# Performance work log

Hardware: AMD Instinct MI355X
Metric: run time of the kernel (lower is better)

Reference implementation:

```python
import jax, jax.numpy as jnp
import numpy as np

N_ITER = 10
TOL = 1e-05
EPS_R = 1e-10
REG = 1e-06
F32_EPS = float(np.finfo(np.float32).eps)


def setup_inputs() -> dict:
    key = jax.random.key(0)
    K, T, F, _ = 6, 2048, 513, 2
    X = jax.random.normal(key, (K, T, F, 2), dtype=jnp.float32)
    return {"X": X}


def _aux_iva_iss(X):
    # X: (K, T, F, 2) real/imag -> complex (F, K, T)
    Xc = (X[..., 0] + 1j * X[..., 1]).astype(jnp.complex64)
    Xc = jnp.transpose(Xc, (2, 0, 1))  # (F, K, T)
    F, K, T = Xc.shape
    eyeK = jnp.eye(K, dtype=jnp.complex64)
    W = jnp.broadcast_to(eyeK, (F, K, K)).astype(jnp.complex64)  # (F, K, K)
    Xh = jnp.conj(Xc)
    done = jnp.array(False)

    for _ in range(N_ITER):
        W_old = W
        # demix: Y[f] = W[f] @ X[f]
        Y = jnp.einsum('fkm,fmt->fkt', W, Xc)
        # per-(source, frame) norms across frequency
        r = jnp.sqrt(jnp.clip(jnp.sum(jnp.abs(Y) ** 2, axis=0), EPS_R))  # (K, T)
        wt = 1.0 / jnp.clip(r, EPS_R)  # laplace contrast g'(r)/r
        # weighted covariances V[f,k] = (X_f * wt[k]) X_f^H / T + reg*I  -> (F, K, K, K)
        V = jnp.einsum('fat,kt,fbt->fkab', Xc, wt.astype(jnp.complex64), Xh) / T
        V = V + REG * eyeK
        # sequential ISS updates over target row k (vectorized over f, m)
        for k in range(K):
            wk = W[:, k, :]  # (F, K)
            wk_c = jnp.conj(wk)
            quad = jnp.einsum('fa,fmab,fb->fm', wk, V, wk_c)  # w_k V_m w_k^H
            denom = jnp.clip(quad.real, EPS_R)  # (F, K)
            num = jnp.einsum('fma,fmab,fb->fm', W, V, wk_c)  # w_m V_m w_k^H
            vk = num / denom  # (F, K)
            vk = vk.at[:, k].set((1.0 - 1.0 / jnp.sqrt(denom[:, k])).astype(jnp.complex64))
            W = W - vk[:, :, None] * wk[:, None, :]
        # emulate early-break on relative change (freeze W once converged)
        W = jnp.where(done, W_old, W)
        diff = jnp.linalg.norm((W - W_old).reshape(-1))
        rel = diff / jnp.clip(jnp.linalg.norm(W_old.reshape(-1)), F32_EPS)
        done = jnp.logical_or(done, rel < TOL)

    Y = jnp.einsum('fkm,fmt->fkt', W, Xc)  # (F, K, T)
    # ref_mic == 0 -> no projection-back rescaling
    Y_out = jnp.transpose(Y, (1, 2, 0))  # (K, T, F)
    return jnp.stack([Y_out.real, Y_out.imag], axis=-1)  # (K, T, F, 2)


def reference(X):
    return _aux_iva_iss(X)
```

## Files before the change

kernel.cpp:

```cpp
#include <hip/hip_runtime.h>
#include <hip/hip_bf16.h>
#include <math.h>

#define T_DIM 2048
#define F_DIM 513
#define N_ITER 10

#define OFF_W0   0
#define OFF_W1   36936
#define OFF_P0   73872
#define OFF_P1   74898
#define OFF_RA0  75924
#define OFF_RA1  88212
#define OFF_VP   100500

typedef __attribute__((ext_vector_type(8))) short bf16x8;
typedef __attribute__((ext_vector_type(4))) float f32x4;

static __device__ inline unsigned pack2bf(float a, float b) {
    union { __hip_bfloat16 h; unsigned short u; } ca, cb;
    ca.h = __float2bfloat16(a);
    cb.h = __float2bfloat16(b);
    return (unsigned)ca.u | ((unsigned)cb.u << 16);
}

static __device__ inline void scatterV(float* V6, int e, float sum) {
    if (e < 6) {
        V6[(e * 6 + e) * 2]     = sum + 1e-6f;
        V6[(e * 6 + e) * 2 + 1] = 0.f;
    } else if (e < 21) {
        int p = e - 6;
        int a = (p < 1) ? 1 : (p < 3) ? 2 : (p < 6) ? 3 : (p < 10) ? 4 : 5;
        int b = p - a * (a - 1) / 2;
        V6[(a * 6 + b) * 2] = sum;
        V6[(b * 6 + a) * 2] = sum;
    } else {
        int p = e - 21;
        int a = (p < 1) ? 1 : (p < 3) ? 2 : (p < 6) ? 3 : (p < 10) ? 4 : 5;
        int b = p - a * (a - 1) / 2;
        V6[(a * 6 + b) * 2 + 1] =  sum;
        V6[(b * 6 + a) * 2 + 1] = -sum;
    }
}

__global__ __launch_bounds__(256) void transp(const float2* __restrict__ X,
                                              float2* __restrict__ Xt,
                                              float* __restrict__ ws) {
    const int fb  = blockIdx.x + 64 * (blockIdx.y + 17 * blockIdx.z);
    const int tid = threadIdx.x;
    if (fb < 73) {
        int idx = fb * 256 + tid;
        if (idx < F_DIM * 36) {
            int e = idx % 36;
            ws[OFF_W0 + 2 * idx]     = ((e / 6) == (e % 6)) ? 1.0f : 0.0f;
            ws[OFF_W0 + 2 * idx + 1] = 0.0f;
        }
    } else if (fb < 78) {
        int idx = (fb - 73) * 256 + tid;
        if (idx < 2 * F_DIM) { ws[OFF_P0 + idx] = 1.0f; ws[OFF_P1 + idx] = 1.0f; }
    } else if (fb < 126) {
        int idx = (fb - 78) * 256 + tid;
        if (idx < 12288) ws[OFF_RA0 + idx] = 0.0f;
    }

    __shared__ float2 tile[32][33];
    const int k  = blockIdx.z;
    const int t0 = blockIdx.x * 32;
    const int f0 = blockIdx.y * 32;
    const int tx = tid & 31, ty = tid >> 5;
#pragma unroll
    for (int j = 0; j < 4; ++j) {
        int t = t0 + ty + j * 8;
        int f = f0 + tx;
        if (f < F_DIM) tile[ty + j * 8][tx] = X[((size_t)k * T_DIM + t) * F_DIM + f];
    }
    __syncthreads();
#pragma unroll
    for (int j = 0; j < 4; ++j) {
        int f = f0 + ty + j * 8;
        int t = t0 + tx;
        if (f < F_DIM) Xt[((size_t)f * 6 + k) * T_DIM + t] = tile[tx][ty + j * 8];
    }
}

__global__ __launch_bounds__(256) void passA1C(const float2* __restrict__ Xt,
                                               float* __restrict__ ws,
                                               const float* __restrict__ pin,
                                               float* __restrict__ pout,
                                               const float* __restrict__ wOld,
                                               float* __restrict__ wNew,
                                               float* __restrict__ r2acc,
                                               int do_iss) {
    __shared__ float Wl[16][72];
    __shared__ float VL[16][432];
    __shared__ float sc[8];
    const int tid = threadIdx.x, wv = tid >> 6, lane = tid & 63;
    const int tc = blockIdx.x, fc = blockIdx.y;

    bool frozen;
    {
        float d2 = 0.f, o2 = 0.f;
        for (int i = tid; i < F_DIM; i += 256) { d2 += pin[2 * i]; o2 += pin[2 * i + 1]; }
#pragma unroll
        for (int d = 1; d < 64; d <<= 1) { d2 += __shfl_xor(d2, d); o2 += __shfl_xor(o2, d); }
        if (lane == 0) { sc[wv * 2] = d2; sc[wv * 2 + 1] = o2; }
        __syncthreads();
        d2 = sc[0] + sc[2] + sc[4] + sc[6];
        o2 = sc[1] + sc[3] + sc[5] + sc[7];
        float rel = sqrtf(d2) / fmaxf(sqrtf(o2), 1.1920929e-07f);
        frozen = (rel < 1e-5f);
        __syncthreads();
    }

    const int fl = wv * 4 + (lane >> 4);
    const int f  = fc * 16 + fl;
    const int m  = lane & 15;
    const bool act = (f < F_DIM) && (m < 6);

    if (do_iss == 0) {
        if (act) {
            const float* Wp = wOld + ((size_t)f * 36 + m * 6) * 2;
#pragma unroll
            for (int a = 0; a < 6; ++a) {
                Wl[fl][(m * 6 + a) * 2]     = Wp[2 * a];
                Wl[fl][(m * 6 + a) * 2 + 1] = Wp[2 * a + 1];
            }
        }
    } else if (frozen) {
        if (act) {
            const float* Wp = wOld + ((size_t)f * 36 + m * 6) * 2;
            float* Wq = wNew + ((size_t)f * 36 + m * 6) * 2;
#pragma unroll
            for (int a = 0; a < 6; ++a) {
                float v0 = Wp[2 * a], v1 = Wp[2 * a + 1];
                Wq[2 * a] = v0; Wq[2 * a + 1] = v1;
                Wl[fl][(m * 6 + a) * 2] = v0; Wl[fl][(m * 6 + a) * 2 + 1] = v1;
            }
        }
        if (tc == 0 && m == 0 && f < F_DIM) { pout[2 * f] = 0.f; pout[2 * f + 1] = 1.f; }
    } else {
        if (f < F_DIM) {
            const float* vp = ws + OFF_VP + (size_t)f * 4 * 216;
            for (int v = m; v < 216; v += 16) {
                float sum = (vp[v] + vp[216 + v] + vp[432 + v] + vp[648 + v]) * (1.0f / (float)T_DIM);
                scatterV(&VL[fl][(v / 36) * 72], v % 36, sum);
            }
        }
        __syncthreads();
        float w6[6][2], wo6[6][2];
#pragma unroll
        for (int a = 0; a < 6; ++a) { w6[a][0] = 0.f; w6[a][1] = 0.f; wo6[a][0] = 0.f; wo6[a][1] = 0.f; }
        if (act) {
            const float* Wp = wOld + ((size_t)f * 36 + m * 6) * 2;
#pragma unroll
            for (int a = 0; a < 6; ++a) {
                w6[a][0] = Wp[2 * a]; w6[a][1] = Wp[2 * a + 1];
                wo6[a][0] = w6[a][0]; wo6[a][1] = w6[a][1];
            }
        }
        const float2* Vm = (const float2*)&VL[fl][0];
        for (int kk = 0; kk < 6; ++kk) {
            float wk[6][2];
#pragma unroll
            for (int a = 0; a < 6; ++a) {
                wk[a][0] = __shfl(w6[a][0], kk, 16);
                wk[a][1] = __shfl(w6[a][1], kk, 16);
            }
            if (act) {
                float t6[6][2];
#pragma unroll
                for (int a = 0; a < 6; ++a) {
                    float tr = 0.f, ti = 0.f;
#pragma unroll
                    for (int b = 0; b < 6; ++b) {
                        float2 vv = Vm[m * 36 + a * 6 + b];
                        tr += vv.x * wk[b][0] + vv.y * wk[b][1];
                        ti += vv.y * wk[b][0] - vv.x * wk[b][1];
                    }
                    t6[a][0] = tr; t6[a][1] = ti;
                }
                float quad = 0.f, nr = 0.f, ni = 0.f;
#pragma unroll
                for (int a = 0; a < 6; ++a) {
                    quad += wk[a][0] * t6[a][0] - wk[a][1] * t6[a][1];
                    nr   += w6[a][0] * t6[a][0] - w6[a][1] * t6[a][1];
                    ni   += w6[a][0] * t6[a][1] + w6[a][1] * t6[a][0];
                }
                float denom = fmaxf(quad, 1e-10f);
                float vkr, vki;
                if (m == kk) { vkr = 1.0f - 1.0f / sqrtf(denom); vki = 0.0f; }
                else { float inv = 1.0f / denom; vkr = nr * inv; vki = ni * inv; }
#pragma unroll
                for (int a = 0; a < 6; ++a) {
                    w6[a][0] -= vkr * wk[a][0] - vki * wk[a][1];
                    w6[a][1] -= vkr * wk[a][1] + vki * wk[a][0];
                }
            }
        }
        float d2 = 0.f, o2 = 0.f;
        if (act) {
            float* Wq = wNew + ((size_t)f * 36 + m * 6) * 2;
#pragma unroll
            for (int a = 0; a < 6; ++a) {
                Wq[2 * a] = w6[a][0]; Wq[2 * a + 1] = w6[a][1];
                Wl[fl][(m * 6 + a) * 2] = w6[a][0]; Wl[fl][(m * 6 + a) * 2 + 1] = w6[a][1];
                float dr = w6[a][0] - wo6[a][0], di = w6[a][1] - wo6[a][1];
                d2 += dr * dr + di * di;
                o2 += wo6[a][0] * wo6[a][0] + wo6[a][1] * wo6[a][1];
            }
        }
#pragma unroll
        for (int d = 1; d < 8; d <<= 1) {
            d2 += __shfl_xor(d2, d);
            o2 += __shfl_xor(o2, d);
        }
        if (tc == 0 && m == 0 && f < F_DIM) { pout[2 * f] = d2; pout[2 * f + 1] = o2; }
    }
    __syncthreads();
    if (do_iss && frozen) return;

    float* r2s = &VL[0][0];
    const int t2 = tc * 128 + lane * 2;
    float acc[6][2];
#pragma unroll
    for (int k = 0; k < 6; ++k) { acc[k][0] = 0.f; acc[k][1] = 0.f; }
#pragma unroll
    for (int i = 0; i < 4; ++i) {
        const int ff = fc * 16 + wv * 4 + i;
        if (ff < F_DIM) {
            const float2* xf = Xt + (size_t)ff * 6 * T_DIM;
            float4 x4[6];
#pragma unroll
            for (int mm = 0; mm < 6; ++mm)
                x4[mm] = *(const float4*)(xf + (size_t)mm * T_DIM + t2);
            const float* wrow = Wl[wv * 4 + i];
#pragma unroll
            for (int k = 0; k < 6; ++k) {
                float y0r = 0.f, y0i = 0.f, y1r = 0.f, y1i = 0.f;
#pragma unroll
                for (int mm = 0; mm < 6; ++mm) {
                    float wr = wrow[(k * 6 + mm) * 2], wi = wrow[(k * 6 + mm) * 2 + 1];
                    y0r += wr * x4[mm].x - wi * x4[mm].y;
                    y0i += wr * x4[mm].y + wi * x4[mm].x;
                    y1r += wr * x4[mm].z - wi * x4[mm].w;
                    y1i += wr * x4[mm].w + wi * x4[mm].z;
                }
                acc[k][0] += y0r * y0r + y0i * y0i;
                acc[k][1] += y1r * y1r + y1i * y1i;
            }
        }
    }
    __syncthreads();
#pragma unroll
    for (int k = 0; k < 6; ++k) {
        r2s[(wv * 6 + k) * 128 + lane * 2]     = acc[k][0];
        r2s[(wv * 6 + k) * 128 + lane * 2 + 1] = acc[k][1];
    }
    __syncthreads();
    for (int v = tid; v < 768; v += 256) {
        int k = v >> 7, l = v & 127;
        float s = r2s[(0 * 6 + k) * 128 + l] + r2s[(1 * 6 + k) * 128 + l]
                + r2s[(2 * 6 + k) * 128 + l] + r2s[(3 * 6 + k) * 128 + l];
        atomicAdd(&r2acc[k * T_DIM + tc * 128 + l], s);
    }
}

__global__ __launch_bounds__(384) void passB(const float2* __restrict__ Xt,
                                             float* __restrict__ ws,
                                             const float* __restrict__ pin,
                                             const float* __restrict__ r2in,
                                             float* __restrict__ r2zero) {
    __shared__ __align__(16) char plane[16 * 528];
    __shared__ __align__(16) float gbuf[6][256];
    __shared__ float sc[12];
    const int tid = threadIdx.x, wv = tid >> 6, lane = tid & 63;
    const int f = blockIdx.x, tq = blockIdx.y;

    {
        float d2 = 0.f, o2 = 0.f;
        for (int i = tid; i < F_DIM; i += 384) { d2 += pin[2 * i]; o2 += pin[2 * i + 1]; }
#pragma unroll
        for (int d = 1; d < 64; d <<= 1) { d2 += __shfl_xor(d2, d); o2 += __shfl_xor(o2, d); }
        if (lane == 0) { sc[wv * 2] = d2; sc[wv * 2 + 1] = o2; }
        __syncthreads();
        d2 = 0.f; o2 = 0.f;
#pragma unroll
        for (int w = 0; w < 6; ++w) { d2 += sc[w * 2]; o2 += sc[w * 2 + 1]; }
        float rel = sqrtf(d2) / fmaxf(sqrtf(o2), 1.1920929e-07f);
        __syncthreads();
        if (rel < 1e-5f) return;
    }

    {
        int bb = (f * 4 + tq) * 6;
#pragma unroll
        for (int i = 0; i < 6; ++i) {
            int idx = bb + i;
            if (idx < 12288) r2zero[idx] = 0.f;
        }
    }

    const float2* xb = Xt + (size_t)f * 6 * T_DIM;

    for (int i = tid; i < 528; i += 384) ((unsigned*)(plane + 12 * 528))[i] = 0;

    f32x4 acc0 = {0.f, 0.f, 0.f, 0.f};
    f32x4 acc1 = {0.f, 0.f, 0.f, 0.f};
    const int rc = lane & 15;
    const int G  = lane >> 4;
    const char* pu = plane + rc * 528 + G * 16;
    const float* gk = &gbuf[wv][0] + G * 8;

    for (int c = 0; c < 2; ++c) {
        const int t0 = tq * 512 + c * 256;
        __syncthreads();
        for (int i = tid; i < 1536; i += 384) {
            int kk = i >> 8, toff = i & 255;
            float s = r2in[kk * T_DIM + t0 + toff];
            float r = sqrtf(fmaxf(s, 1e-10f));
            gbuf[kk][toff] = 1.0f / fmaxf(r, 1e-10f);
        }
        for (int it = tid; it < 768; it += 384) {
            int mm = it >> 7, q = it & 127;
            float4 xv = *(const float4*)(xb + (size_t)mm * T_DIM + t0 + 2 * q);
            *(unsigned*)(plane + mm * 528 + 4 * q)       = pack2bf(xv.x, xv.z);
            *(unsigned*)(plane + (6 + mm) * 528 + 4 * q) = pack2bf(xv.y, xv.w);
        }
        __syncthreads();
#pragma unroll
        for (int s = 0; s < 8; ++s) {
            bf16x8 b = *(const bf16x8*)(pu + s * 64);
            f32x4 gA = *(const f32x4*)(gk + s * 32);
            f32x4 gB = *(const f32x4*)(gk + s * 32 + 4);
            const unsigned* bu = (const unsigned*)&b;
            bf16x8 a;
            unsigned* au = (unsigned*)&a;
            au[0] = pack2bf(__uint_as_float(bu[0] << 16) * gA[0],
                            __uint_as_float(bu[0] & 0xffff0000u) * gA[1]);
            au[1] = pack2bf(__uint_as_float(bu[1] << 16) * gA[2],
                            __uint_as_float(bu[1] & 0xffff0000u) * gA[3]);
            au[2] = pack2bf(__uint_as_float(bu[2] << 16) * gB[0],
                            __uint_as_float(bu[2] & 0xffff0000u) * gB[1]);
            au[3] = pack2bf(__uint_as_float(bu[3] << 16) * gB[2],
                            __uint_as_float(bu[3] & 0xffff0000u) * gB[3]);
            if (s & 1) acc1 = __builtin_amdgcn_mfma_f32_16x16x32_bf16(a, b, acc1, 0, 0, 0);
            else       acc0 = __builtin_amdgcn_mfma_f32_16x16x32_bf16(a, b, acc0, 0, 0, 0);
        }
    }
    __syncthreads();

    float* S = (float*)plane;
    {
        float* Sk = S + wv * 256;
#pragma unroll
        for (int r = 0; r < 4; ++r)
            Sk[(4 * G + r) * 16 + rc] = acc0[r] + acc1[r];
    }
    __syncthreads();

    if (tid < 216) {
        const int kk = tid / 36, e = tid % 36;
        const float* Sk = S + kk * 256;
        float val;
        if (e < 6) {
            val = Sk[e * 16 + e] + Sk[(6 + e) * 16 + (6 + e)];
        } else if (e < 21) {
            int p = e - 6;
            int a = (p < 1) ? 1 : (p < 3) ? 2 : (p < 6) ? 3 : (p < 10) ? 4 : 5;
            int b = p - a * (a - 1) / 2;
            val = Sk[a * 16 + b] + Sk[(6 + a) * 16 + (6 + b)];
        } else {
            int p = e - 21;
            int a = (p < 1) ? 1 : (p < 3) ? 2 : (p < 6) ? 3 : (p < 10) ? 4 : 5;
            int b = p - a * (a - 1) / 2;
            val = Sk[(6 + a) * 16 + b] - Sk[a * 16 + (6 + b)];
        }
        ws[OFF_VP + ((size_t)f * 4 + tq) * 216 + tid] = val;
    }
}

__global__ __launch_bounds__(64) void passC(float* __restrict__ ws,
                                            const float* __restrict__ pin,
                                            float* __restrict__ pout,
                                            const float* __restrict__ wOld,
                                            float* __restrict__ wNew) {
    __shared__ float VL[432];
    const int f = blockIdx.x;
    const int lane = threadIdx.x;
    {
        float d2 = 0.f, o2 = 0.f;
        for (int i = lane; i < F_DIM; i += 64) { d2 += pin[2 * i]; o2 += pin[2 * i + 1]; }
#pragma unroll
        for (int d = 1; d < 64; d <<= 1) { d2 += __shfl_xor(d2, d); o2 += __shfl_xor(o2, d); }
        float rel = sqrtf(d2) / fmaxf(sqrtf(o2), 1.1920929e-07f);
        if (rel < 1e-5f) {
            for (int v = lane; v < 72; v += 64)
                wNew[(size_t)f * 72 + v] = wOld[(size_t)f * 72 + v];
            if (lane == 0) { pout[2 * f] = 0.0f; pout[2 * f + 1] = 1.0f; }
            return;
        }
    }
    {
        const float* vp = ws + OFF_VP + (size_t)f * 4 * 216;
        for (int v = lane; v < 216; v += 64) {
            float sum = (vp[v] + vp[216 + v] + vp[432 + v] + vp[648 + v]) * (1.0f / (float)T_DIM);
            scatterV(&VL[(v / 36) * 72], v % 36, sum);
        }
    }
    __syncthreads();

    const int m = lane;
    const bool act = (m < 6);
    float w6[6][2], wo6[6][2];
#pragma unroll
    for (int a = 0; a < 6; ++a) { w6[a][0] = 0.f; w6[a][1] = 0.f; wo6[a][0] = 0.f; wo6[a][1] = 0.f; }
    if (act) {
        const float* Wp = wOld + ((size_t)f * 36 + m * 6) * 2;
#pragma unroll
        for (int a = 0; a < 6; ++a) {
            w6[a][0] = Wp[2 * a]; w6[a][1] = Wp[2 * a + 1];
            wo6[a][0] = w6[a][0]; wo6[a][1] = w6[a][1];
        }
    }
    const float2* Vm = (const float2*)VL;
    for (int kk = 0; kk < 6; ++kk) {
        float wk[6][2];
#pragma unroll
        for (int a = 0; a < 6; ++a) {
            wk[a][0] = __shfl(w6[a][0], kk);
            wk[a][1] = __shfl(w6[a][1], kk);
        }
        if (act) {
            float t6[6][2];
#pragma unroll
            for (int a = 0; a < 6; ++a) {
                float tr = 0.f, ti = 0.f;
#pragma unroll
                for (int b = 0; b < 6; ++b) {
                    float2 vv = Vm[m * 36 + a * 6 + b];
                    tr += vv.x * wk[b][0] + vv.y * wk[b][1];
                    ti += vv.y * wk[b][0] - vv.x * wk[b][1];
                }
                t6[a][0] = tr; t6[a][1] = ti;
            }
            float quad = 0.f, nr = 0.f, ni = 0.f;
#pragma unroll
            for (int a = 0; a < 6; ++a) {
                quad += wk[a][0] * t6[a][0] - wk[a][1] * t6[a][1];
                nr   += w6[a][0] * t6[a][0] - w6[a][1] * t6[a][1];
                ni   += w6[a][0] * t6[a][1] + w6[a][1] * t6[a][0];
            }
            float denom = fmaxf(quad, 1e-10f);
            float vkr, vki;
            if (m == kk) { vkr = 1.0f - 1.0f / sqrtf(denom); vki = 0.0f; }
            else { float inv = 1.0f / denom; vkr = nr * inv; vki = ni * inv; }
#pragma unroll
            for (int a = 0; a < 6; ++a) {
                w6[a][0] -= vkr * wk[a][0] - vki * wk[a][1];
                w6[a][1] -= vkr * wk[a][1] + vki * wk[a][0];
            }
        }
    }
    float d2 = 0.f, o2 = 0.f;
    if (act) {
        float* Wq = wNew + ((size_t)f * 36 + m * 6) * 2;
#pragma unroll
        for (int a = 0; a < 6; ++a) {
            Wq[2 * a] = w6[a][0]; Wq[2 * a + 1] = w6[a][1];
            float dr = w6[a][0] - wo6[a][0], di = w6[a][1] - wo6[a][1];
            d2 += dr * dr + di * di;
            o2 += wo6[a][0] * wo6[a][0] + wo6[a][1] * wo6[a][1];
        }
    }
#pragma unroll
    for (int d = 1; d < 8; d <<= 1) {
        d2 += __shfl_xor(d2, d);
        o2 += __shfl_xor(o2, d);
    }
    if (lane == 0) {
        pout[2 * f]     = d2;
        pout[2 * f + 1] = o2;
    }
}

__global__ __launch_bounds__(256) void finalY(const float2* __restrict__ X,
                                              const float* __restrict__ ws,
                                              float2* __restrict__ out) {
    const int f  = blockIdx.y * 256 + threadIdx.x;
    const int t0 = blockIdx.x * 4;
    if (f >= F_DIM) return;
    const float2* Wf = (const float2*)(ws + OFF_W0) + (size_t)f * 36;
    float2 w[36];
#pragma unroll
    for (int i = 0; i < 36; ++i) w[i] = Wf[i];
#pragma unroll
    for (int tl = 0; tl < 4; ++tl) {
        int t = t0 + tl;
        float2 x[6];
#pragma unroll
        for (int m = 0; m < 6; ++m) x[m] = X[((size_t)m * T_DIM + t) * F_DIM + f];
#pragma unroll
        for (int k = 0; k < 6; ++k) {
            float yr = 0.f, yi = 0.f;
#pragma unroll
            for (int m = 0; m < 6; ++m) {
                float2 wk = w[k * 6 + m];
                yr += wk.x * x[m].x - wk.y * x[m].y;
                yi += wk.x * x[m].y + wk.y * x[m].x;
            }
            out[((size_t)k * T_DIM + t) * F_DIM + f] = make_float2(yr, yi);
        }
    }
}

extern "C" void kernel_launch(void* const* d_in, const int* in_sizes, int n_in,
                              void* d_out, int out_size, void* d_ws, size_t ws_size,
                              hipStream_t stream) {
    (void)in_sizes; (void)n_in; (void)out_size; (void)ws_size;
    const float2* X = (const float2*)d_in[0];
    float* ws = (float*)d_ws;
    float2* out = (float2*)d_out;
    float2* Xt = out;

    float* P[2]  = {ws + OFF_P0,  ws + OFF_P1};
    float* W[2]  = {ws + OFF_W0,  ws + OFF_W1};
    float* RA[2] = {ws + OFF_RA0, ws + OFF_RA1};

    transp<<<dim3(64, 17, 6), 256, 0, stream>>>(X, Xt, ws);
    for (int it = 0; it < N_ITER; ++it) {
        const float* wOld = (it == 0) ? W[0] : W[(it + 1) & 1];
        float* wNew = W[it & 1];
        passA1C<<<dim3(16, 33), 256, 0, stream>>>(Xt, ws, P[it & 1], P[(it + 1) & 1],
                                                  wOld, wNew, RA[it & 1], it > 0);
        passB<<<dim3(F_DIM, 4), 384, 0, stream>>>(Xt, ws, P[(it + 1) & 1],
                                                  RA[it & 1], RA[(it + 1) & 1]);
    }
    passC<<<F_DIM, 64, 0, stream>>>(ws, P[0], P[1], W[1], W[0]);
    finalY<<<dim3(T_DIM / 4, 3), 256, 0, stream>>>(X, ws, out);
}
```

Before: 594.9 us.

## Double-buffer passB staging with fewer time splits and widen passA1C to 512 threads

passB now handles 1024 time frames per block, split over 2 blocks per frequency instead of 4. It prefetches the next chunk's X and weights into registers while the MFMA work runs on the current chunk, with a double-buffered LDS plane and weight buffer. This halves the partial covariance outputs the ISS stage has to sum. passA1C is launched with 512 threads, so each wave reduces 2 frequencies in the Y-norm accumulation, while only the first 256 threads do the ISS update. The aims are to hide global-load latency in passB and cut per-block serial work in passA1C, at the cost of fewer passB blocks, more LDS use, and idle threads during the ISS phase.

Result: slower. 682.4 us (+14.7%).

```diff
diff --git a/kernel.cpp b/kernel.cpp
--- a/kernel.cpp
+++ b/kernel.cpp
@@ -83,7 +83,7 @@
     }
 }
 
-__global__ __launch_bounds__(256) void passA1C(const float2* __restrict__ Xt,
+__global__ __launch_bounds__(512) void passA1C(const float2* __restrict__ Xt,
                                                float* __restrict__ ws,
                                                const float* __restrict__ pin,
                                                float* __restrict__ pout,
@@ -93,20 +93,21 @@
                                                int do_iss) {
     __shared__ float Wl[16][72];
     __shared__ float VL[16][432];
-    __shared__ float sc[8];
+    __shared__ float sc[16];
     const int tid = threadIdx.x, wv = tid >> 6, lane = tid & 63;
     const int tc = blockIdx.x, fc = blockIdx.y;
 
     bool frozen;
     {
         float d2 = 0.f, o2 = 0.f;
-        for (int i = tid; i < F_DIM; i += 256) { d2 += pin[2 * i]; o2 += pin[2 * i + 1]; }
+        for (int i = tid; i < F_DIM; i += 512) { d2 += pin[2 * i]; o2 += pin[2 * i + 1]; }
 #pragma unroll
         for (int d = 1; d < 64; d <<= 1) { d2 += __shfl_xor(d2, d); o2 += __shfl_xor(o2, d); }
         if (lane == 0) { sc[wv * 2] = d2; sc[wv * 2 + 1] = o2; }
         __syncthreads();
-        d2 = sc[0] + sc[2] + sc[4] + sc[6];
-        o2 = sc[1] + sc[3] + sc[5] + sc[7];
+        d2 = 0.f; o2 = 0.f;
+#pragma unroll
+        for (int w = 0; w < 8; ++w) { d2 += sc[w * 2]; o2 += sc[w * 2 + 1]; }
         float rel = sqrtf(d2) / fmaxf(sqrtf(o2), 1.1920929e-07f);
         frozen = (rel < 1e-5f);
         __syncthreads();
@@ -115,7 +116,7 @@
     const int fl = wv * 4 + (lane >> 4);
     const int f  = fc * 16 + fl;
     const int m  = lane & 15;
-    const bool act = (f < F_DIM) && (m < 6);
+    const bool act = (tid < 256) && (f < F_DIM) && (m < 6);
 
     if (do_iss == 0) {
         if (act) {
@@ -134,87 +135,90 @@
             for (int a = 0; a < 6; ++a) {
                 float v0 = Wp[2 * a], v1 = Wp[2 * a + 1];
                 Wq[2 * a] = v0; Wq[2 * a + 1] = v1;
-                Wl[fl][(m * 6 + a) * 2] = v0; Wl[fl][(m * 6 + a) * 2 + 1] = v1;
-            }
-        }
-        if (tc == 0 && m == 0 && f < F_DIM) { pout[2 * f] = 0.f; pout[2 * f + 1] = 1.f; }
+            }
+        }
+        if (tid < 256 && tc == 0 && m == 0 && f < F_DIM) {
+            pout[2 * f] = 0.f; pout[2 * f + 1] = 1.f;
+        }
     } else {
-        if (f < F_DIM) {
-            const float* vp = ws + OFF_VP + (size_t)f * 4 * 216;
+        if (tid < 256 && f < F_DIM) {
+            const float* vp = ws + OFF_VP + (size_t)f * 2 * 216;
             for (int v = m; v < 216; v += 16) {
-                float sum = (vp[v] + vp[216 + v] + vp[432 + v] + vp[648 + v]) * (1.0f / (float)T_DIM);
+                float sum = (vp[v] + vp[216 + v]) * (1.0f / (float)T_DIM);
                 scatterV(&VL[fl][(v / 36) * 72], v % 36, sum);
             }
         }
         __syncthreads();
-        float w6[6][2], wo6[6][2];
-#pragma unroll
-        for (int a = 0; a < 6; ++a) { w6[a][0] = 0.f; w6[a][1] = 0.f; wo6[a][0] = 0.f; wo6[a][1] = 0.f; }
-        if (act) {
-            const float* Wp = wOld + ((size_t)f * 36 + m * 6) * 2;
-#pragma unroll
-            for (int a = 0; a < 6; ++a) {
-                w6[a][0] = Wp[2 * a]; w6[a][1] = Wp[2 * a + 1];
-                wo6[a][0] = w6[a][0]; wo6[a][1] = w6[a][1];
-            }
-        }
-        const float2* Vm = (const float2*)&VL[fl][0];
-        for (int kk = 0; kk < 6; ++kk) {
-            float wk[6][2];
-#pragma unroll
-            for (int a = 0; a < 6; ++a) {
-                wk[a][0] = __shfl(w6[a][0], kk, 16);
-                wk[a][1] = __shfl(w6[a][1], kk, 16);
-            }
+        if (tid < 256) {
+            float w6[6][2], wo6[6][2];
+#pragma unroll
+            for (int a = 0; a < 6; ++a) { w6[a][0] = 0.f; w6[a][1] = 0.f; wo6[a][0] = 0.f; wo6[a][1] = 0.f; }
             if (act) {
-                float t6[6][2];
+                const float* Wp = wOld + ((size_t)f * 36 + m * 6) * 2;
 #pragma unroll
                 for (int a = 0; a < 6; ++a) {
-                    float tr = 0.f, ti = 0.f;
-#pragma unroll
-                    for (int b = 0; b < 6; ++b) {
-                        float2 vv = Vm[m * 36 + a * 6 + b];
-                        tr += vv.x * wk[b][0] + vv.y * wk[b][1];
-                        ti += vv.y * wk[b][0] - vv.x * wk[b][1];
+                    w6[a][0] = Wp[2 * a]; w6[a][1] = Wp[2 * a + 1];
+                    wo6[a][0] = w6[a][0]; wo6[a][1] = w6[a][1];
+                }
+            }
+            const float2* Vm = (const float2*)&VL[fl][0];
+            for (int kk = 0; kk < 6; ++kk) {
+                float wk[6][2];
+#pragma unroll
+                for (int a = 0; a < 6; ++a) {
+                    wk[a][0] = __shfl(w6[a][0], kk, 16);
+                    wk[a][1] = __shfl(w6[a][1], kk, 16);
+                }
+                if (act) {
+                    float t6[6][2];
+#pragma unroll
+                    for (int a = 0; a < 6; ++a) {
+                        float tr = 0.f, ti = 0.f;
+#pragma unroll
+                        for (int b = 0; b < 6; ++b) {
+                            float2 vv = Vm[m * 36 + a * 6 + b];
+                            tr += vv.x * wk[b][0] + vv.y * wk[b][1];
+                            ti += vv.y * wk[b][0] - vv.x * wk[b][1];
+                        }
+                        t6[a][0] = tr; t6[a][1] = ti;
                     }
-                    t6[a][0] = tr; t6[a][1] = ti;
+                    float quad = 0.f, nr = 0.f, ni = 0.f;
+#pragma unroll
+                    for (int a = 0; a < 6; ++a) {
+                        quad += wk[a][0] * t6[a][0] - wk[a][1] * t6[a][1];
+                        nr   += w6[a][0] * t6[a][0] - w6[a][1] * t6[a][1];
+                        ni   += w6[a][0] * t6[a][1] + w6[a][1] * t6[a][0];
+                    }
+                    float denom = fmaxf(quad, 1e-10f);
+                    float vkr, vki;
+                    if (m == kk) { vkr = 1.0f - 1.0f / sqrtf(denom); vki = 0.0f; }
+                    else { float inv = 1.0f / denom; vkr = nr * inv; vki = ni * inv; }
+#pragma unroll
+                    for (int a = 0; a < 6; ++a) {
+                        w6[a][0] -= vkr * wk[a][0] - vki * wk[a][1];
+                        w6[a][1] -= vkr * wk[a][1] + vki * wk[a][0];
+                    }
                 }
-                float quad = 0.f, nr = 0.f, ni = 0.f;
+            }
+            float d2 = 0.f, o2 = 0.f;
+            if (act) {
+                float* Wq = wNew + ((size_t)f * 36 + m * 6) * 2;
 #pragma unroll
                 for (int a = 0; a < 6; ++a) {
-                    quad += wk[a][0] * t6[a][0] - wk[a][1] * t6[a][1];
-                    nr   += w6[a][0] * t6[a][0] - w6[a][1] * t6[a][1];
-                    ni   += w6[a][0] * t6[a][1] + w6[a][1] * t6[a][0];
+                    Wq[2 * a] = w6[a][0]; Wq[2 * a + 1] = w6[a][1];
+                    Wl[fl][(m * 6 + a) * 2] = w6[a][0]; Wl[fl][(m * 6 + a) * 2 + 1] = w6[a][1];
+                    float dr = w6[a][0] - wo6[a][0], di = w6[a][1] - wo6[a][1];
+                    d2 += dr * dr + di * di;
+                    o2 += wo6[a][0] * wo6[a][0] + wo6[a][1] * wo6[a][1];
                 }
-                float denom = fmaxf(quad, 1e-10f);
-                float vkr, vki;
-                if (m == kk) { vkr = 1.0f - 1.0f / sqrtf(denom); vki = 0.0f; }
-                else { float inv = 1.0f / denom; vkr = nr * inv; vki = ni * inv; }
-#pragma unroll
-                for (int a = 0; a < 6; ++a) {
-                    w6[a][0] -= vkr * wk[a][0] - vki * wk[a][1];
-                    w6[a][1] -= vkr * wk[a][1] + vki * wk[a][0];
-                }
-            }
-        }
-        float d2 = 0.f, o2 = 0.f;
-        if (act) {
-            float* Wq = wNew + ((size_t)f * 36 + m * 6) * 2;
-#pragma unroll
-            for (int a = 0; a < 6; ++a) {
-                Wq[2 * a] = w6[a][0]; Wq[2 * a + 1] = w6[a][1];
-                Wl[fl][(m * 6 + a) * 2] = w6[a][0]; Wl[fl][(m * 6 + a) * 2 + 1] = w6[a][1];
-                float dr = w6[a][0] - wo6[a][0], di = w6[a][1] - wo6[a][1];
-                d2 += dr * dr + di * di;
-                o2 += wo6[a][0] * wo6[a][0] + wo6[a][1] * wo6[a][1];
-            }
-        }
-#pragma unroll
-        for (int d = 1; d < 8; d <<= 1) {
-            d2 += __shfl_xor(d2, d);
-            o2 += __shfl_xor(o2, d);
-        }
-        if (tc == 0 && m == 0 && f < F_DIM) { pout[2 * f] = d2; pout[2 * f + 1] = o2; }
+            }
+#pragma unroll
+            for (int d = 1; d < 8; d <<= 1) {
+                d2 += __shfl_xor(d2, d);
+                o2 += __shfl_xor(o2, d);
+            }
+            if (tc == 0 && m == 0 && f < F_DIM) { pout[2 * f] = d2; pout[2 * f + 1] = o2; }
+        }
     }
     __syncthreads();
     if (do_iss && frozen) return;
@@ -225,15 +229,15 @@
 #pragma unroll
     for (int k = 0; k < 6; ++k) { acc[k][0] = 0.f; acc[k][1] = 0.f; }
 #pragma unroll
-    for (int i = 0; i < 4; ++i) {
-        const int ff = fc * 16 + wv * 4 + i;
+    for (int i = 0; i < 2; ++i) {
+        const int ff = fc * 16 + wv * 2 + i;
         if (ff < F_DIM) {
             const float2* xf = Xt + (size_t)ff * 6 * T_DIM;
             float4 x4[6];
 #pragma unroll
             for (int mm = 0; mm < 6; ++mm)
                 x4[mm] = *(const float4*)(xf + (size_t)mm * T_DIM + t2);
-            const float* wrow = Wl[wv * 4 + i];
+            const float* wrow = Wl[wv * 2 + i];
 #pragma unroll
             for (int k = 0; k < 6; ++k) {
                 float y0r = 0.f, y0i = 0.f, y1r = 0.f, y1i = 0.f;
@@ -250,17 +254,17 @@
             }
         }
     }
-    __syncthreads();
 #pragma unroll
     for (int k = 0; k < 6; ++k) {
         r2s[(wv * 6 + k) * 128 + lane * 2]     = acc[k][0];
         r2s[(wv * 6 + k) * 128 + lane * 2 + 1] = acc[k][1];
     }
     __syncthreads();
-    for (int v = tid; v < 768; v += 256) {
+    for (int v = tid; v < 768; v += 512) {
         int k = v >> 7, l = v & 127;
-        float s = r2s[(0 * 6 + k) * 128 + l] + r2s[(1 * 6 + k) * 128 + l]
-                + r2s[(2 * 6 + k) * 128 + l] + r2s[(3 * 6 + k) * 128 + l];
+        float s = 0.f;
+#pragma unroll
+        for (int w = 0; w < 8; ++w) s += r2s[(w * 6 + k) * 128 + l];
         atomicAdd(&r2acc[k * T_DIM + tc * 128 + l], s);
     }
 }
@@ -270,8 +274,8 @@
                                              const float* __restrict__ pin,
                                              const float* __restrict__ r2in,
                                              float* __restrict__ r2zero) {
-    __shared__ __align__(16) char plane[16 * 528];
-    __shared__ __align__(16) float gbuf[6][256];
+    __shared__ __align__(16) char plane[2][16 * 528];
+    __shared__ __align__(16) float gbuf[2][6][256];
     __shared__ float sc[12];
     const int tid = threadIdx.x, wv = tid >> 6, lane = tid & 63;
     const int f = blockIdx.x, tq = blockIdx.y;
@@ -292,9 +296,9 @@
     }
 
     {
-        int bb = (f * 4 + tq) * 6;
-#pragma unroll
-        for (int i = 0; i < 6; ++i) {
+        int bb = (f * 2 + tq) * 12;
+#pragma unroll
+        for (int i = 0; i < 12; ++i) {
             int idx = bb + i;
             if (idx < 12288) r2zero[idx] = 0.f;
         }
@@ -302,31 +306,54 @@
 
     const float2* xb = Xt + (size_t)f * 6 * T_DIM;
 
-    for (int i = tid; i < 528; i += 384) ((unsigned*)(plane + 12 * 528))[i] = 0;
+    for (int i = tid; i < 1056; i += 384) {
+        int b = i / 528, j = i % 528;
+        ((unsigned*)(plane[b] + 12 * 528))[j] = 0;
+    }
+
+    const int m0 = tid >> 7, q0 = tid & 127;
+    const int m1 = (tid + 384) >> 7, q1 = (tid + 384) & 127;
+
+    {
+        const int t0 = tq * 1024;
+#pragma unroll
+        for (int j = 0; j < 4; ++j) {
+            int idx = tid + j * 384;
+            int kk = idx >> 8, toff = idx & 255;
+            float s = r2in[kk * T_DIM + t0 + toff];
+            float r = sqrtf(fmaxf(s, 1e-10f));
+            gbuf[0][kk][toff] = 1.0f / fmaxf(r, 1e-10f);
+        }
+        float4 xv0 = *(const float4*)(xb + (size_t)m0 * T_DIM + t0 + 2 * q0);
+        float4 xv1 = *(const float4*)(xb + (size_t)m1 * T_DIM + t0 + 2 * q1);
+        *(unsigned*)(plane[0] + m0 * 528 + 4 * q0)       = pack2bf(xv0.x, xv0.z);
+        *(unsigned*)(plane[0] + (6 + m0) * 528 + 4 * q0) = pack2bf(xv0.y, xv0.w);
+        *(unsigned*)(plane[0] + m1 * 528 + 4 * q1)       = pack2bf(xv1.x, xv1.z);
+        *(unsigned*)(plane[0] + (6 + m1) * 528 + 4 * q1) = pack2bf(xv1.y, xv1.w);
+    }
+    __syncthreads();
 
     f32x4 acc0 = {0.f, 0.f, 0.f, 0.f};
     f32x4 acc1 = {0.f, 0.f, 0.f, 0.f};
     const int rc = lane & 15;
     const int G  = lane >> 4;
-    const char* pu = plane + rc * 528 + G * 16;
-    const float* gk = &gbuf[wv][0] + G * 8;
-
-    for (int c = 0; c < 2; ++c) {
-        const int t0 = tq * 512 + c * 256;
-        __syncthreads();
-        for (int i = tid; i < 1536; i += 384) {
-            int kk = i >> 8, toff = i & 255;
-            float s = r2in[kk * T_DIM + t0 + toff];
-            float r = sqrtf(fmaxf(s, 1e-10f));
-            gbuf[kk][toff] = 1.0f / fmaxf(r, 1e-10f);
-        }
-        for (int it = tid; it < 768; it += 384) {
-            int mm = it >> 7, q = it & 127;
-            float4 xv = *(const float4*)(xb + (size_t)mm * T_DIM + t0 + 2 * q);
-            *(unsigned*)(plane + mm * 528 + 4 * q)       = pack2bf(xv.x, xv.z);
-            *(unsigned*)(plane + (6 + mm) * 528 + 4 * q) = pack2bf(xv.y, xv.w);
-        }
-        __syncthreads();
+
+    for (int c = 0; c < 4; ++c) {
+        const int buf = c & 1;
+        float4 px0, px1;
+        float pg[4];
+        if (c < 3) {
+            const int tn = tq * 1024 + (c + 1) * 256;
+#pragma unroll
+            for (int j = 0; j < 4; ++j) {
+                int idx = tid + j * 384;
+                pg[j] = r2in[(idx >> 8) * T_DIM + tn + (idx & 255)];
+            }
+            px0 = *(const float4*)(xb + (size_t)m0 * T_DIM + tn + 2 * q0);
+            px1 = *(const float4*)(xb + (size_t)m1 * T_DIM + tn + 2 * q1);
+        }
+        const char* pu = plane[buf] + rc * 528 + G * 16;
+        const float* gk = &gbuf[buf][wv][0] + G * 8;
 #pragma unroll
         for (int s = 0; s < 8; ++s) {
             bf16x8 b = *(const bf16x8*)(pu + s * 64);
@@ -346,10 +373,24 @@
             if (s & 1) acc1 = __builtin_amdgcn_mfma_f32_16x16x32_bf16(a, b, acc1, 0, 0, 0);
             else       acc0 = __builtin_amdgcn_mfma_f32_16x16x32_bf16(a, b, acc0, 0, 0, 0);
         }
-    }
-    __syncthreads();
-
-    float* S = (float*)plane;
+        if (c < 3) {
+            const int nbuf = buf ^ 1;
+#pragma unroll
+            for (int j = 0; j < 4; ++j) {
+                int idx = tid + j * 384;
+                float r = sqrtf(fmaxf(pg[j], 1e-10f));
+                gbuf[nbuf][idx >> 8][idx & 255] = 1.0f / fmaxf(r, 1e-10f);
+            }
+            *(unsigned*)(plane[nbuf] + m0 * 528 + 4 * q0)       = pack2bf(px0.x, px0.z);
+            *(unsigned*)(plane[nbuf] + (6 + m0) * 528 + 4 * q0) = pack2bf(px0.y, px0.w);
+            *(unsigned*)(plane[nbuf] + m1 * 528 + 4 * q1)       = pack2bf(px1.x, px1.z);
+            *(unsigned*)(plane[nbuf] + (6 + m1) * 528 + 4 * q1) = pack2bf(px1.y, px1.w);
+            __syncthreads();
+        }
+    }
+    __syncthreads();
+
+    float* S = (float*)plane[0];
     {
         float* Sk = S + wv * 256;
 #pragma unroll
@@ -375,7 +416,7 @@
             int b = p - a * (a - 1) / 2;
             val = Sk[(6 + a) * 16 + b] - Sk[a * 16 + (6 + b)];
         }
-        ws[OFF_VP + ((size_t)f * 4 + tq) * 216 + tid] = val;
+        ws[OFF_VP + ((size_t)f * 2 + tq) * 216 + tid] = val;
     }
 }
 
@@ -401,9 +442,9 @@
         }
     }
     {
-        const float* vp = ws + OFF_VP + (size_t)f * 4 * 216;
+        const float* vp = ws + OFF_VP + (size_t)f * 2 * 216;
         for (int v = lane; v < 216; v += 64) {
-            float sum = (vp[v] + vp[216 + v] + vp[432 + v] + vp[648 + v]) * (1.0f / (float)T_DIM);
+            float sum = (vp[v] + vp[216 + v]) * (1.0f / (float)T_DIM);
             scatterV(&VL[(v / 36) * 72], v % 36, sum);
         }
     }
@@ -530,9 +571,9 @@
     for (int it = 0; it < N_ITER; ++it) {
         const float* wOld = (it == 0) ? W[0] : W[(it + 1) & 1];
         float* wNew = W[it & 1];
-        passA1C<<<dim3(16, 33), 256, 0, stream>>>(Xt, ws, P[it & 1], P[(it + 1) & 1],
+        passA1C<<<dim3(16, 33), 512, 0, stream>>>(Xt, ws, P[it & 1], P[(it + 1) & 1],
                                                   wOld, wNew, RA[it & 1], it > 0);
-        passB<<<dim3(F_DIM, 4), 384, 0, stream>>>(Xt, ws, P[(it + 1) & 1],
+        passB<<<dim3(F_DIM, 2), 384, 0, stream>>>(Xt, ws, P[(it + 1) & 1],
                                                   RA[it & 1], RA[(it + 1) & 1]);
     }
     passC<<<F_DIM, 64, 0, stream>>>(ws, P[0], P[1], W[1], W[0]);
```

## Pre-scale X by sqrt of weights per source to form symmetric Gram MFMA

Applied to the files above, without the earlier changes.

Instead of scaling one MFMA operand by the weight inside the inner loop (unpack bf16, multiply, repack), each source k gets its own LDS plane holding X scaled by sqrt(weight), so the covariance becomes A*A^T with a single LDS load per step. This removes per-lane unpack/scale/pack work from the MFMA loop. In exchange it multiplies LDS usage by six, adds a barrier and six times more packing writes during staging, and adds sqrt rounding before bf16 quantization.

Result: slower. 925.0 us (+55.5%).

```diff
diff --git a/kernel.cpp b/kernel.cpp
--- a/kernel.cpp
+++ b/kernel.cpp
@@ -270,8 +270,8 @@
                                              const float* __restrict__ pin,
                                              const float* __restrict__ r2in,
                                              float* __restrict__ r2zero) {
-    __shared__ __align__(16) char plane[16 * 528];
-    __shared__ __align__(16) float gbuf[6][256];
+    __shared__ __align__(16) char plane[6][16 * 528];
+    __shared__ __align__(16) float sgbuf[6][256];
     __shared__ float sc[12];
     const int tid = threadIdx.x, wv = tid >> 6, lane = tid & 63;
     const int f = blockIdx.x, tq = blockIdx.y;
@@ -302,14 +302,16 @@
 
     const float2* xb = Xt + (size_t)f * 6 * T_DIM;
 
-    for (int i = tid; i < 528; i += 384) ((unsigned*)(plane + 12 * 528))[i] = 0;
+    for (int i = tid; i < 3168; i += 384) {
+        int p = i / 528, off = i % 528;
+        *(unsigned*)(plane[p] + 12 * 528 + 4 * off) = 0;
+    }
 
     f32x4 acc0 = {0.f, 0.f, 0.f, 0.f};
     f32x4 acc1 = {0.f, 0.f, 0.f, 0.f};
     const int rc = lane & 15;
     const int G  = lane >> 4;
-    const char* pu = plane + rc * 528 + G * 16;
-    const float* gk = &gbuf[wv][0] + G * 8;
+    const char* pk = plane[wv] + rc * 528 + G * 16;
 
     for (int c = 0; c < 2; ++c) {
         const int t0 = tq * 512 + c * 256;
@@ -318,38 +320,30 @@
             int kk = i >> 8, toff = i & 255;
             float s = r2in[kk * T_DIM + t0 + toff];
             float r = sqrtf(fmaxf(s, 1e-10f));
-            gbuf[kk][toff] = 1.0f / fmaxf(r, 1e-10f);
-        }
-        for (int it = tid; it < 768; it += 384) {
-            int mm = it >> 7, q = it & 127;
+            sgbuf[kk][toff] = sqrtf(1.0f / fmaxf(r, 1e-10f));
+        }
+        __syncthreads();
+        for (int it2 = tid; it2 < 768; it2 += 384) {
+            int mm = it2 >> 7, q = it2 & 127;
             float4 xv = *(const float4*)(xb + (size_t)mm * T_DIM + t0 + 2 * q);
-            *(unsigned*)(plane + mm * 528 + 4 * q)       = pack2bf(xv.x, xv.z);
-            *(unsigned*)(plane + (6 + mm) * 528 + 4 * q) = pack2bf(xv.y, xv.w);
+#pragma unroll
+            for (int k = 0; k < 6; ++k) {
+                float g0 = sgbuf[k][2 * q], g1 = sgbuf[k][2 * q + 1];
+                *(unsigned*)(plane[k] + mm * 528 + 4 * q)       = pack2bf(g0 * xv.x, g1 * xv.z);
+                *(unsigned*)(plane[k] + (6 + mm) * 528 + 4 * q) = pack2bf(g0 * xv.y, g1 * xv.w);
+            }
         }
         __syncthreads();
 #pragma unroll
         for (int s = 0; s < 8; ++s) {
-            bf16x8 b = *(const bf16x8*)(pu + s * 64);
-            f32x4 gA = *(const f32x4*)(gk + s * 32);
-            f32x4 gB = *(const f32x4*)(gk + s * 32 + 4);
-            const unsigned* bu = (const unsigned*)&b;
-            bf16x8 a;
-            unsigned* au = (unsigned*)&a;
-            au[0] = pack2bf(__uint_as_float(bu[0] << 16) * gA[0],
-                            __uint_as_float(bu[0] & 0xffff0000u) * gA[1]);
-            au[1] = pack2bf(__uint_as_float(bu[1] << 16) * gA[2],
-                            __uint_as_float(bu[1] & 0xffff0000u) * gA[3]);
-            au[2] = pack2bf(__uint_as_float(bu[2] << 16) * gB[0],
-                            __uint_as_float(bu[2] & 0xffff0000u) * gB[1]);
-            au[3] = pack2bf(__uint_as_float(bu[3] << 16) * gB[2],
-                            __uint_as_float(bu[3] & 0xffff0000u) * gB[3]);
-            if (s & 1) acc1 = __builtin_amdgcn_mfma_f32_16x16x32_bf16(a, b, acc1, 0, 0, 0);
-            else       acc0 = __builtin_amdgcn_mfma_f32_16x16x32_bf16(a, b, acc0, 0, 0, 0);
-        }
-    }
-    __syncthreads();
-
-    float* S = (float*)plane;
+            bf16x8 a = *(const bf16x8*)(pk + s * 64);
+            if (s & 1) acc1 = __builtin_amdgcn_mfma_f32_16x16x32_bf16(a, a, acc1, 0, 0, 0);
+            else       acc0 = __builtin_amdgcn_mfma_f32_16x16x32_bf16(a, a, acc0, 0, 0, 0);
+        }
+    }
+    __syncthreads();
+
+    float* S = (float*)plane[0];
     {
         float* Sk = S + wv * 256;
 #pragma unroll
```
